# Optimization experiments

Hardware: AMD Instinct MI355X
Metric: run time of the kernel (lower is better)

Reference implementation:

```python
import jax, jax.numpy as jnp
import numpy as np

B, PP, LP, H = 128, 1024, 128, 256  # graphs, protein atoms/graph, ligand atoms/graph, hidden
NP, NL = B * PP, B * LP


def setup_inputs() -> dict:
    key = jax.random.key(0)
    ks = jax.random.split(key, 16)
    s = 0.02
    return {
        "protein_pos": 10.0 * jax.random.normal(ks[0], (NP, 3), jnp.float32),
        "ligand_pos": 10.0 * jax.random.normal(ks[1], (NL, 3), jnp.float32),
        "protein_element": jax.random.randint(ks[2], (NP,), 0, 128),
        "protein_aa": jax.random.randint(ks[3], (NP,), 0, 32),
        "protein_is_backbone": jax.random.randint(ks[4], (NP,), 0, 2),
        "ligand_type": jax.random.randint(ks[5], (NL,), 0, 16),
        "protein_batch": jnp.repeat(jnp.arange(B), PP),  # block-contiguous segments
        "ligand_batch": jnp.repeat(jnp.arange(B), LP),
        "E_elem": s * jax.random.normal(ks[6], (128, H), jnp.float32),
        "E_aa": s * jax.random.normal(ks[7], (32, H), jnp.float32),
        "E_bb": s * jax.random.normal(ks[8], (2, H), jnp.float32),
        "E_lig": s * jax.random.normal(ks[9], (16, H), jnp.float32),
        "Wd1": s * jax.random.normal(ks[10], (H, H), jnp.float32),
        "bd1": jnp.zeros((H,), jnp.float32),
        "Wd2": s * jax.random.normal(ks[11], (H, H), jnp.float32),
        "bd2": jnp.zeros((H,), jnp.float32),
        "Wa1": s * jax.random.normal(ks[12], (2 * H + 2, H), jnp.float32),
        "ba1": jnp.zeros((H,), jnp.float32),
        "Wa2": s * jax.random.normal(ks[13], (H, 1), jnp.float32),
        "ba2": jnp.zeros((1,), jnp.float32),
    }


def _pool_by_batch(x, batch, bsz):
    # mean-pool rows of x into bsz segments (index_add_ + bincount in torch)
    summed = jax.ops.segment_sum(x, batch, num_segments=bsz)
    counts = jax.ops.segment_sum(jnp.ones((x.shape[0],), x.dtype), batch, num_segments=bsz)
    return summed / jnp.maximum(counts, 1.0)[:, None]


def reference(protein_pos, ligand_pos, protein_element, protein_aa, protein_is_backbone,
              ligand_type, protein_batch, ligand_batch,
              E_elem, E_aa, E_bb, E_lig, Wd1, bd1, Wd2, bd2, Wa1, ba1, Wa2, ba2):
    # protein / ligand node embeddings
    h_protein = E_elem[protein_element] + E_aa[protein_aa] + E_bb[protein_is_backbone]
    h_ligand = E_lig[ligand_type]

    # compose_context: protein first, then ligand (mask_ligand = [0]*NP + [1]*NL)
    h_ctx = jnp.concatenate([h_protein, h_ligand], axis=0)

    # stub denoiser: pointwise 2-layer SiLU MLP producing out['h']
    h_out = jax.nn.silu(h_ctx @ Wd1 + bd1) @ Wd2 + bd2
    protein_h = h_out[:protein_pos.shape[0]]
    ligand_h = h_out[protein_pos.shape[0]:]

    pooled_protein = _pool_by_batch(protein_h, protein_batch, B)  # [B, H]
    pooled_ligand = _pool_by_batch(ligand_h, ligand_batch, B)     # [B, H]

    # contact features: per-graph cdist(lig, prot), min over protein atoms,
    # then mean & min over ligand atoms. Uniform block layout -> dense reshape.
    prot = protein_pos.reshape(B, PP, 3)
    lig = ligand_pos.reshape(B, LP, 3)
    d2 = jnp.sum((lig[:, :, None, :] - prot[:, None, :, :]) ** 2, axis=-1)  # [B, LP, PP]
    dist = jnp.sqrt(d2)
    min_lp = dist.min(axis=2)                                    # [B, LP]
    contact = jnp.stack([min_lp.mean(axis=1), min_lp.min(axis=1)], axis=-1)  # [B, 2]

    graph_feat = jnp.concatenate([pooled_protein, pooled_ligand, contact], axis=-1)  # [B, 2H+2]
    affinity = (jax.nn.silu(graph_feat @ Wa1 + ba1) @ Wa2 + ba2).squeeze(-1)  # [B]
    return affinity
```

## Files before the change

### kernel.cpp

```cpp
#include <hip/hip_runtime.h>
#include <hip/hip_bf16.h>

typedef _Float16 f16;
typedef _Float16 h4 __attribute__((ext_vector_type(4)));
typedef float f32x4 __attribute__((ext_vector_type(4)));

#define B_   128
#define PP_  1024
#define LP_  128
#define H_   256
#define NP_  131072
#define NL_  16384


__global__ void __launch_bounds__(256) tbl_k(
    const float* __restrict__ W1,
    const float* __restrict__ Ee, const float* __restrict__ Ea,
    const float* __restrict__ Eb, const float* __restrict__ El,
    const float* __restrict__ bd1,
    f16* __restrict__ tbl, float* __restrict__ ysum)
{
  __shared__ float src[256];
  const int bid = blockIdx.x, tid = threadIdx.x;
  ysum[bid * 256 + tid] = 0.f;
  if (bid >= 178) return;

  const float* s;
  float badd = 0.f;
  if (bid < 128)      s = Ee + bid * 256;
  else if (bid < 160) s = Ea + (bid - 128) * 256;
  else if (bid < 162) { s = Eb + (bid - 160) * 256; badd = bd1[tid]; }
  else                { s = El + (bid - 162) * 256; badd = bd1[tid]; }
  src[tid] = s[tid];
  __syncthreads();
  float a0 = 0.f, a1 = 0.f, a2 = 0.f, a3 = 0.f;
#pragma unroll 4
  for (int k = 0; k < 256; k += 4) {
    a0 += src[k]     * W1[(k)     * 256 + tid];
    a1 += src[k + 1] * W1[(k + 1) * 256 + tid];
    a2 += src[k + 2] * W1[(k + 2) * 256 + tid];
    a3 += src[k + 3] * W1[(k + 3) * 256 + tid];
  }
  tbl[bid * 256 + tid] = (f16)(((a0 + a1) + (a2 + a3)) + badd);
}

__global__ void __launch_bounds__(256, 4) mid_k(
    const float* __restrict__ W2, const float* __restrict__ Wa1,
    const float* __restrict__ ba1, const float* __restrict__ bd2,
    const float* __restrict__ ppos, const float* __restrict__ lpos,
    const int* __restrict__ pel, const int* __restrict__ paa,
    const int* __restrict__ pbb, const int* __restrict__ ltyp,
    const f16* __restrict__ tbl,
    float* __restrict__ wc, float* __restrict__ cvec,
    float* __restrict__ gmin, float* __restrict__ ysum)
{
  __shared__ __align__(16) float sm[1536];
  const int bid = blockIdx.x, tid = threadIdx.x;

  if (bid < 512) {
    const int half = bid >> 8, rr = bid & 255;
    sm[tid] = W2[rr * 256 + tid];
    __syncthreads();
    const float* W = Wa1 + half * 65536 + tid;
    float a0 = 0.f, a1 = 0.f, a2 = 0.f, a3 = 0.f;
#pragma unroll 4
    for (int n = 0; n < 256; n += 4) {
      a0 += sm[n]     * W[(n)     * 256];
      a1 += sm[n + 1] * W[(n + 1) * 256];
      a2 += sm[n + 2] * W[(n + 2) * 256];
      a3 += sm[n + 3] * W[(n + 3) * 256];
    }
    const float scale = half ? (1.f / (float)LP_) : (1.f / (float)PP_);
    wc[half * 65536 + rr * 256 + tid] = ((a0 + a1) + (a2 + a3)) * scale;

  } else if (bid == 512) {
    float a = ba1[tid];
#pragma unroll 8
    for (int n = 0; n < 256; ++n)
      a += bd2[n] * (Wa1[n * 256 + tid] + Wa1[(256 + n) * 256 + tid]);
    cvec[tid] = a;

  } else if (bid < 769) {
    const int cb = bid - 513, b = cb >> 1, half = cb & 1;
    float* px = sm;
    float* py = sm + 512;
    float* pz = sm + 1024;
#pragma unroll
    for (int r = 0; r < 2; ++r) {
      const int i = r * 256 + tid;
      const float* p = ppos + ((size_t)b * PP_ + half * 512 + i) * 3;
      px[i] = p[0]; py[i] = p[1]; pz[i] = p[2];
    }
    __syncthreads();
    const int lig = tid >> 1, part = tid & 1;
    const float* lp = lpos + ((size_t)b * LP_ + lig) * 3;
    const float lx = lp[0], ly = lp[1], lz = lp[2];
    const float4* X4 = (const float4*)(px + part * 256);
    const float4* Y4 = (const float4*)(py + part * 256);
    const float4* Z4 = (const float4*)(pz + part * 256);
    float m = 3.4e38f;
#pragma unroll 4
    for (int i = 0; i < 64; ++i) {
      float4 X = X4[i], Y = Y4[i], Z = Z4[i];
      float dx, dy, dz, d2;
      dx = lx - X.x; dy = ly - Y.x; dz = lz - Z.x;
      d2 = dx * dx + dy * dy + dz * dz; m = fminf(m, d2);
      dx = lx - X.y; dy = ly - Y.y; dz = lz - Z.y;
      d2 = dx * dx + dy * dy + dz * dz; m = fminf(m, d2);
      dx = lx - X.z; dy = ly - Y.z; dz = lz - Z.z;
      d2 = dx * dx + dy * dy + dz * dz; m = fminf(m, d2);
      dx = lx - X.w; dy = ly - Y.w; dz = lz - Z.w;
      d2 = dx * dx + dy * dy + dz * dz; m = fminf(m, d2);
    }
    m = fminf(m, __shfl_xor(m, 1));
    if (!part) gmin[cb * 128 + lig] = m;

  } else {
    const int idx = bid - 769;
    const int batch = idx / 18, g = idx % 18;
    const int wave = tid >> 6, lane = tid & 63;
    const int c0 = lane * 4;
    f32x4 acc = (f32x4){0.f, 0.f, 0.f, 0.f};

    if (g < 16) {
      const int base = batch * PP_ + g * 64 + wave * 16;
#pragma unroll 4
      for (int r = 0; r < 16; ++r) {
        const int i = base + r;
        h4 va = *(const h4*)(tbl + pel[i] * 256 + c0);
        h4 vb = *(const h4*)(tbl + 32768 + paa[i] * 256 + c0);
        h4 vc = *(const h4*)(tbl + 40960 + pbb[i] * 256 + c0);
#pragma unroll
        for (int k = 0; k < 4; ++k) {
          float pre = (float)va[k] + (float)vb[k] + (float)vc[k];
          acc[k] += pre * __builtin_amdgcn_rcpf(1.f + __expf(-pre));
        }
      }
    } else {
      const int base = batch * LP_ + (g - 16) * 64 + wave * 16;
#pragma unroll 4
      for (int r = 0; r < 16; ++r) {
        const int i = base + r;
        h4 v = *(const h4*)(tbl + 41472 + ltyp[i] * 256 + c0);
#pragma unroll
        for (int k = 0; k < 4; ++k) {
          float pre = (float)v[k];
          acc[k] += pre * __builtin_amdgcn_rcpf(1.f + __expf(-pre));
        }
      }
    }

    f32x4* red = (f32x4*)sm;
    if (wave) red[(wave - 1) * 64 + lane] = acc;
    __syncthreads();
    if (wave == 0) {
      f32x4 a1 = red[lane], a2 = red[64 + lane], a3 = red[128 + lane];
      float* pool = ysum + (g < 16 ? 0 : 32768) + batch * 256 + c0;
#pragma unroll
      for (int k = 0; k < 4; ++k)
        atomicAdd(pool + k, ((acc[k] + a1[k]) + (a2[k] + a3[k])));
    }
  }
}

__global__ void __launch_bounds__(512) head_k(
    const float* __restrict__ ysum, const float* __restrict__ wc,
    const float* __restrict__ cvec, const float* __restrict__ Wa1,
    const float* __restrict__ Wa2, const float* __restrict__ ba2,
    const float* __restrict__ gmin, float* __restrict__ out)
{
  __shared__ float ysc[512];
  __shared__ float part[512];
  __shared__ float lmin[128];
  __shared__ float cls[2];
  __shared__ float red[4];
  const int b = blockIdx.x, tid = threadIdx.x;

  ysc[tid] = (tid < 256) ? ysum[b * 256 + tid]
                         : ysum[32768 + b * 256 + (tid - 256)];
  if (tid < 128) {
    const float m = fminf(gmin[(b * 2) * 128 + tid], gmin[(b * 2 + 1) * 128 + tid]);
    lmin[tid] = sqrtf(m);
  }
  __syncthreads();

  if (tid < 64) {
    const float a0 = lmin[tid], a1 = lmin[tid + 64];
    float sm = a0 + a1, mn = fminf(a0, a1);
#pragma unroll
    for (int off = 32; off; off >>= 1) {
      sm += __shfl_down(sm, off);
      mn = fminf(mn, __shfl_down(mn, off));
    }
    if (tid == 0) { cls[0] = sm * (1.f / (float)LP_); cls[1] = mn; }
  }

  {
    const int gg = tid >> 8, j = tid & 255;
    const float* W = wc + gg * 65536 + j;
    const float* ys = ysc + gg * 256;
    float a[8];
#pragma unroll
    for (int u = 0; u < 8; ++u) a[u] = 0.f;
#pragma unroll 2
    for (int k = 0; k < 256; k += 8) {
#pragma unroll
      for (int u = 0; u < 8; ++u)
        a[u] += ys[k + u] * W[(k + u) * 256];
    }
    part[tid] = ((a[0] + a[1]) + (a[2] + a[3])) + ((a[4] + a[5]) + (a[6] + a[7]));
  }
  __syncthreads();

  if (tid < 256) {
    float pre = part[tid] + part[256 + tid] + cvec[tid]
              + cls[0] * Wa1[512 * 256 + tid] + cls[1] * Wa1[513 * 256 + tid];
    float si = pre * __builtin_amdgcn_rcpf(1.f + __expf(-pre));
    float p = si * Wa2[tid];
#pragma unroll
    for (int off = 32; off; off >>= 1) p += __shfl_down(p, off);
    if ((tid & 63) == 0) red[tid >> 6] = p;
  }
  __syncthreads();
  if (tid == 0) out[b] = (red[0] + red[1]) + (red[2] + red[3]) + ba2[0];
}

extern "C" void kernel_launch(void* const* d_in, const int* in_sizes, int n_in,
                              void* d_out, int out_size, void* d_ws, size_t ws_size,
                              hipStream_t stream)
{
  const float* protein_pos = (const float*)d_in[0];
  const float* ligand_pos  = (const float*)d_in[1];
  const int*   pel  = (const int*)d_in[2];
  const int*   paa  = (const int*)d_in[3];
  const int*   pbb  = (const int*)d_in[4];
  const int*   ltyp = (const int*)d_in[5];
  const float* Ee  = (const float*)d_in[8];
  const float* Ea  = (const float*)d_in[9];
  const float* Eb  = (const float*)d_in[10];
  const float* El  = (const float*)d_in[11];
  const float* Wd1 = (const float*)d_in[12];
  const float* bd1 = (const float*)d_in[13];
  const float* Wd2 = (const float*)d_in[14];
  const float* bd2 = (const float*)d_in[15];
  const float* Wa1 = (const float*)d_in[16];
  const float* ba1 = (const float*)d_in[17];
  const float* Wa2 = (const float*)d_in[18];
  const float* ba2 = (const float*)d_in[19];
  float* out = (float*)d_out;

  char* ws = (char*)d_ws;
  f16*   tbl  = (f16*)(ws);
  float* ysum = (float*)(ws + 98304);
  float* wc   = (float*)(ws + 360448);
  float* cvec = (float*)(ws + 884736);
  float* gmin = (float*)(ws + 885760);

  tbl_k<<<256, 256, 0, stream>>>(Wd1, Ee, Ea, Eb, El, bd1, tbl, ysum);
  mid_k<<<3073, 256, 0, stream>>>(Wd2, Wa1, ba1, bd2, protein_pos, ligand_pos,
                                  pel, paa, pbb, ltyp, tbl, wc, cvec, gmin, ysum);
  head_k<<<B_, 512, 0, stream>>>(ysum, wc, cvec, Wa1, Wa2, ba2, gmin, out);
}
```

Baseline: 131.2 us.

## Register-block weight matmuls across rows and split head over output halves

The embedding-table kernel now computes two table rows per block, and the Wd2·Wa1 fold kernel computes eight rows per block. Each loaded weight element is reused across several rows in registers, which cuts global weight traffic and the block count in the mid kernel. The head kernel is split into two 256-thread blocks per graph, each handling half of the hidden outputs, and they combine their partial results with an atomicAdd into an output that the table kernel now zeroes. In exchange the head kernel relies on atomics and on a zeroing write made in an earlier launch, and fewer, longer blocks do the folded weight work.

```diff
diff --git a/kernel.cpp b/kernel.cpp
--- a/kernel.cpp
+++ b/kernel.cpp
@@ -18,30 +18,34 @@
     const float* __restrict__ Ee, const float* __restrict__ Ea,
     const float* __restrict__ Eb, const float* __restrict__ El,
     const float* __restrict__ bd1,
-    f16* __restrict__ tbl, float* __restrict__ ysum)
-{
-  __shared__ float src[256];
+    f16* __restrict__ tbl, float* __restrict__ ysum, float* __restrict__ out)
+{
+  __shared__ float s0[256], s1[256];
   const int bid = blockIdx.x, tid = threadIdx.x;
   ysum[bid * 256 + tid] = 0.f;
-  if (bid >= 178) return;
-
+  if (bid == 90 && tid < 128) out[tid] = 0.f;
+  if (bid >= 89) return;
+
+  const int r0 = bid * 2;
   const float* s;
   float badd = 0.f;
-  if (bid < 128)      s = Ee + bid * 256;
-  else if (bid < 160) s = Ea + (bid - 128) * 256;
-  else if (bid < 162) { s = Eb + (bid - 160) * 256; badd = bd1[tid]; }
-  else                { s = El + (bid - 162) * 256; badd = bd1[tid]; }
-  src[tid] = s[tid];
-  __syncthreads();
-  float a0 = 0.f, a1 = 0.f, a2 = 0.f, a3 = 0.f;
-#pragma unroll 4
-  for (int k = 0; k < 256; k += 4) {
-    a0 += src[k]     * W1[(k)     * 256 + tid];
-    a1 += src[k + 1] * W1[(k + 1) * 256 + tid];
-    a2 += src[k + 2] * W1[(k + 2) * 256 + tid];
-    a3 += src[k + 3] * W1[(k + 3) * 256 + tid];
-  }
-  tbl[bid * 256 + tid] = (f16)(((a0 + a1) + (a2 + a3)) + badd);
+  if (r0 < 128)      s = Ee + r0 * 256;
+  else if (r0 < 160) s = Ea + (r0 - 128) * 256;
+  else if (r0 < 162) { s = Eb + (r0 - 160) * 256; badd = bd1[tid]; }
+  else               { s = El + (r0 - 162) * 256; badd = bd1[tid]; }
+  s0[tid] = s[tid];
+  s1[tid] = s[256 + tid];
+  __syncthreads();
+  float a0 = 0.f, a1 = 0.f, b0 = 0.f, b1 = 0.f;
+#pragma unroll 4
+  for (int k = 0; k < 256; k += 2) {
+    const float w0 = W1[(k)     * 256 + tid];
+    const float w1 = W1[(k + 1) * 256 + tid];
+    a0 += s0[k] * w0;     b0 += s0[k + 1] * w1;
+    a1 += s1[k] * w0;     b1 += s1[k + 1] * w1;
+  }
+  tbl[r0 * 256 + tid]       = (f16)(a0 + b0 + badd);
+  tbl[(r0 + 1) * 256 + tid] = (f16)(a1 + b1 + badd);
 }
 
 __global__ void __launch_bounds__(256, 4) mid_k(
@@ -54,34 +58,38 @@
     float* __restrict__ wc, float* __restrict__ cvec,
     float* __restrict__ gmin, float* __restrict__ ysum)
 {
-  __shared__ __align__(16) float sm[1536];
+  __shared__ __align__(16) float sm[2048];
   const int bid = blockIdx.x, tid = threadIdx.x;
 
-  if (bid < 512) {
-    const int half = bid >> 8, rr = bid & 255;
-    sm[tid] = W2[rr * 256 + tid];
+  if (bid < 64) {
+    const int half = bid >> 5, r0 = (bid & 31) * 8;
+#pragma unroll
+    for (int r = 0; r < 8; ++r) sm[r * 256 + tid] = W2[(r0 + r) * 256 + tid];
     __syncthreads();
     const float* W = Wa1 + half * 65536 + tid;
-    float a0 = 0.f, a1 = 0.f, a2 = 0.f, a3 = 0.f;
-#pragma unroll 4
-    for (int n = 0; n < 256; n += 4) {
-      a0 += sm[n]     * W[(n)     * 256];
-      a1 += sm[n + 1] * W[(n + 1) * 256];
-      a2 += sm[n + 2] * W[(n + 2) * 256];
-      a3 += sm[n + 3] * W[(n + 3) * 256];
+    float a[8];
+#pragma unroll
+    for (int r = 0; r < 8; ++r) a[r] = 0.f;
+#pragma unroll 4
+    for (int n = 0; n < 256; ++n) {
+      const float w = W[n * 256];
+#pragma unroll
+      for (int r = 0; r < 8; ++r) a[r] += sm[r * 256 + n] * w;
     }
     const float scale = half ? (1.f / (float)LP_) : (1.f / (float)PP_);
-    wc[half * 65536 + rr * 256 + tid] = ((a0 + a1) + (a2 + a3)) * scale;
-
-  } else if (bid == 512) {
+#pragma unroll
+    for (int r = 0; r < 8; ++r)
+      wc[half * 65536 + (r0 + r) * 256 + tid] = a[r] * scale;
+
+  } else if (bid == 64) {
     float a = ba1[tid];
 #pragma unroll 8
     for (int n = 0; n < 256; ++n)
       a += bd2[n] * (Wa1[n * 256 + tid] + Wa1[(256 + n) * 256 + tid]);
     cvec[tid] = a;
 
-  } else if (bid < 769) {
-    const int cb = bid - 513, b = cb >> 1, half = cb & 1;
+  } else if (bid < 321) {
+    const int cb = bid - 65, b = cb >> 1, half = cb & 1;
     float* px = sm;
     float* py = sm + 512;
     float* pz = sm + 1024;
@@ -116,7 +124,7 @@
     if (!part) gmin[cb * 128 + lig] = m;
 
   } else {
-    const int idx = bid - 769;
+    const int idx = bid - 321;
     const int batch = idx / 18, g = idx % 18;
     const int wave = tid >> 6, lane = tid & 63;
     const int c0 = lane * 4;
@@ -163,21 +171,21 @@
   }
 }
 
-__global__ void __launch_bounds__(512) head_k(
+__global__ void __launch_bounds__(256) head_k(
     const float* __restrict__ ysum, const float* __restrict__ wc,
     const float* __restrict__ cvec, const float* __restrict__ Wa1,
     const float* __restrict__ Wa2, const float* __restrict__ ba2,
     const float* __restrict__ gmin, float* __restrict__ out)
 {
   __shared__ float ysc[512];
-  __shared__ float part[512];
+  __shared__ float part[256];
   __shared__ float lmin[128];
   __shared__ float cls[2];
-  __shared__ float red[4];
-  const int b = blockIdx.x, tid = threadIdx.x;
-
-  ysc[tid] = (tid < 256) ? ysum[b * 256 + tid]
-                         : ysum[32768 + b * 256 + (tid - 256)];
+  __shared__ float red[2];
+  const int b = blockIdx.x >> 1, jh = blockIdx.x & 1, tid = threadIdx.x;
+
+  ysc[tid]       = ysum[b * 256 + tid];
+  ysc[256 + tid] = ysum[32768 + b * 256 + tid];
   if (tid < 128) {
     const float m = fminf(gmin[(b * 2) * 128 + tid], gmin[(b * 2 + 1) * 128 + tid]);
     lmin[tid] = sqrtf(m);
@@ -196,9 +204,9 @@
   }
 
   {
-    const int gg = tid >> 8, j = tid & 255;
-    const float* W = wc + gg * 65536 + j;
-    const float* ys = ysc + gg * 256;
+    const int kh = tid >> 7, jj = tid & 127;
+    const float* W = wc + kh * 65536 + jh * 128 + jj;
+    const float* ys = ysc + kh * 256;
     float a[8];
 #pragma unroll
     for (int u = 0; u < 8; ++u) a[u] = 0.f;
@@ -212,17 +220,18 @@
   }
   __syncthreads();
 
-  if (tid < 256) {
-    float pre = part[tid] + part[256 + tid] + cvec[tid]
-              + cls[0] * Wa1[512 * 256 + tid] + cls[1] * Wa1[513 * 256 + tid];
+  if (tid < 128) {
+    const int j = jh * 128 + tid;
+    float pre = part[tid] + part[128 + tid] + cvec[j]
+              + cls[0] * Wa1[512 * 256 + j] + cls[1] * Wa1[513 * 256 + j];
     float si = pre * __builtin_amdgcn_rcpf(1.f + __expf(-pre));
-    float p = si * Wa2[tid];
+    float p = si * Wa2[j];
 #pragma unroll
     for (int off = 32; off; off >>= 1) p += __shfl_down(p, off);
     if ((tid & 63) == 0) red[tid >> 6] = p;
   }
   __syncthreads();
-  if (tid == 0) out[b] = (red[0] + red[1]) + (red[2] + red[3]) + ba2[0];
+  if (tid == 0) atomicAdd(out + b, red[0] + red[1] + (jh ? 0.f : ba2[0]));
 }
 
 extern "C" void kernel_launch(void* const* d_in, const int* in_sizes, int n_in,
@@ -256,8 +265,8 @@
   float* cvec = (float*)(ws + 884736);
   float* gmin = (float*)(ws + 885760);
 
-  tbl_k<<<256, 256, 0, stream>>>(Wd1, Ee, Ea, Eb, El, bd1, tbl, ysum);
-  mid_k<<<3073, 256, 0, stream>>>(Wd2, Wa1, ba1, bd2, protein_pos, ligand_pos,
+  tbl_k<<<256, 256, 0, stream>>>(Wd1, Ee, Ea, Eb, El, bd1, tbl, ysum, out);
+  mid_k<<<2625, 256, 0, stream>>>(Wd2, Wa1, ba1, bd2, protein_pos, ligand_pos,
                                   pel, paa, pbb, ltyp, tbl, wc, cvec, gmin, ysum);
-  head_k<<<B_, 512, 0, stream>>>(ysum, wc, cvec, Wa1, Wa2, ba2, gmin, out);
-}
+  head_k<<<256, 256, 0, stream>>>(ysum, wc, cvec, Wa1, Wa2, ba2, gmin, out);
+}
```

Measured after the change: 133.7 us. No clear change (+1.9%).
